# Optimization experiments

Hardware: AMD Instinct MI355X
Metric: run time of the kernel (lower is better)

Reference implementation:

```python
import jax, jax.numpy as jnp
import numpy as np

N_NODES = 50000
N_EDGES = 400000
H, D = 4, 32  # num_heads, per-head dim
NEG_SLOPE = 0.1


def setup_inputs() -> dict:
    key = jax.random.key(0)
    ks = jax.random.split(key, 12)
    inp = {
        'features': jax.random.normal(ks[0], (N_NODES, 256), jnp.float32) * 0.1,
        'src': jax.random.randint(ks[1], (N_EDGES,), 0, N_NODES, jnp.int32),
        'dst': jax.random.randint(ks[2], (N_EDGES,), 0, N_NODES, jnp.int32),
        'w': jax.random.uniform(ks[3], (N_EDGES,), jnp.float32),
        'W1': jax.random.normal(ks[4], (256, 128), jnp.float32) * 0.05,
        'al1': jax.random.normal(ks[5], (H, D), jnp.float32) * 0.1,
        'ar1': jax.random.normal(ks[6], (H, D), jnp.float32) * 0.1,
        'W2': jax.random.normal(ks[7], (128, 128), jnp.float32) * 0.05,
        'al2': jax.random.normal(ks[8], (H, D), jnp.float32) * 0.1,
        'ar2': jax.random.normal(ks[9], (H, D), jnp.float32) * 0.1,
        'Wout': jax.random.normal(ks[10], (256, 128), jnp.float32) * 0.05,
        'bout': jnp.zeros((128,), jnp.float32),
    }
    return inp


def _gat_layer(x, W, al, ar, src, dst, w):
    # x: [N, in_dim] -> ft: [N, H, D]
    ft = (x @ W).reshape(-1, H, D)
    el = jnp.einsum('nhd,hd->nh', ft, al)  # left attention logits per node
    er = jnp.einsum('nhd,hd->nh', ft, ar)
    # edge logits: leaky_relu(el[src] + er[dst]), then edge-weight scaling
    e = jax.nn.leaky_relu(el[src] + er[dst], negative_slope=NEG_SLOPE)  # [E, H]
    e = w[:, None] * e
    # segment softmax over incoming edges of each destination node
    m = jax.ops.segment_max(e, dst, num_segments=N_NODES)  # [N, H]
    a = jnp.exp(e - m[dst])
    s = jax.ops.segment_sum(a, dst, num_segments=N_NODES)
    a = a / s[dst]  # [E, H]
    # weighted scatter-sum aggregation: rst[dst] += a * ft[src]
    msg = ft[src] * a[:, :, None]  # [E, H, D]
    rst = jax.ops.segment_sum(msg, dst, num_segments=N_NODES)  # [N, H, D]
    # activation=relu, then concat heads (contiguous -> reshape)
    return jax.nn.relu(rst).reshape(-1, H * D)


def reference(features, src, dst, w, W1, al1, ar1, W2, al2, ar2, Wout, bout):
    x1 = _gat_layer(features, W1, al1, ar1, src, dst, w)  # [N, 128]
    x2 = _gat_layer(x1, W2, al2, ar2, src, dst, w)        # [N, 128]
    h = jnp.concatenate([x1, x2], axis=-1)                # [N, 256]
    return h @ Wout + bout                                # [N, 128]
```

## Files before the change

kernel.cpp:

```cpp
#include <hip/hip_runtime.h>
#include <math.h>

#define NHEAD 4
#define HDIM 32
#define NEG_SLOPE 0.1f

typedef unsigned short u16;
typedef unsigned int u32;
typedef _Float16 f16;
typedef f16 f16x2 __attribute__((ext_vector_type(2)));
typedef f16 f16x4 __attribute__((ext_vector_type(4)));
typedef f16 f16x8 __attribute__((ext_vector_type(8)));
typedef float f32x4 __attribute__((ext_vector_type(4)));

#define GLLDS16(g, l) __builtin_amdgcn_global_load_lds( \
    (const __attribute__((address_space(1))) void*)(g), \
    (__attribute__((address_space(3))) void*)(l), 16, 0, 0)


__device__ __forceinline__ void cast_panel(const float* __restrict__ W,
                                           const float* __restrict__ al,
                                           const float* __restrict__ ar,
                                           u16* __restrict__ bp, int t, int NC) {
    int per_kt = NC * 16;
    int kt = t / per_kt;
    int rem = t - kt * per_kt;
    int n = rem >> 4;
    int kkp = rem & 15;
    int k = kt * 32 + kkp * 2;
    float v0 = 0.f, v1 = 0.f;
    if (n < 128) {
        v0 = W[(size_t)k * 128 + n];
        v1 = W[(size_t)(k + 1) * 128 + n];
    } else if (n < 136) {
        const float* av = (n < 132) ? al : ar;
        int h = (n < 132) ? (n - 128) : (n - 132);
        float s0 = 0.f, s1 = 0.f;
        for (int d = 0; d < 32; d++) {
            float a = av[h * 32 + d];
            s0 += W[(size_t)k * 128 + h * 32 + d] * a;
            s1 += W[(size_t)(k + 1) * 128 + h * 32 + d] * a;
        }
        v0 = s0; v1 = s1;
    }
    f16x2 p;
    p.x = (f16)v0; p.y = (f16)v1;
    *(f16x2*)&((u32*)bp)[t] = p;
}

__global__ void histcast_k(const int* __restrict__ dst, int* __restrict__ cnt, int E,
                           const float* __restrict__ W1, const float* __restrict__ al1,
                           const float* __restrict__ ar1, u16* __restrict__ b1,
                           const float* __restrict__ W2, const float* __restrict__ al2,
                           const float* __restrict__ ar2, u16* __restrict__ b2,
                           const float* __restrict__ W3, u16* __restrict__ b3) {
    int t = blockIdx.x * 256 + threadIdx.x;
    if (t < E) atomicAdd(&cnt[dst[t]], 1);
    if (t < 18432) cast_panel(W1, al1, ar1, b1, t, 144);
    else if (t < 27648) cast_panel(W2, al2, ar2, b2, t - 18432, 144);
    else if (t < 44032) cast_panel(W3, nullptr, nullptr, b3, t - 27648, 128);
}


__global__ void assign_k(const int* __restrict__ cnt, int* __restrict__ start,
                         int* __restrict__ ctr, int N) {
    __shared__ int s[256];
    __shared__ int base;
    int t = threadIdx.x;
    int i = blockIdx.x * 256 + t;
    int v = (i < N) ? cnt[i] : 0;
    s[t] = v;
    __syncthreads();
    int incl = v;
    for (int off = 1; off < 256; off <<= 1) {
        int add = (t >= off) ? s[t - off] : 0;
        __syncthreads();
        incl += add;
        s[t] = incl;
        __syncthreads();
    }
    if (t == 255) base = atomicAdd(ctr, incl);
    __syncthreads();
    if (i < N) start[i] = base + incl - v;
}

__global__ void scatter_k(const int* __restrict__ src, const int* __restrict__ dst,
                          const float* __restrict__ w, const int* __restrict__ start,
                          int* __restrict__ fill, int2* __restrict__ edge_s, int E) {
    int e = blockIdx.x * 256 + threadIdx.x;
    if (e >= E) return;
    int d = dst[e];
    int p = atomicAdd(&fill[d], 1);
    edge_s[start[d] + p] = make_int2(src[e], __float_as_int(w[e]));
}


template <int NT>
__global__ __launch_bounds__(256) void gemm_h_k(
        const void* __restrict__ Av, int a_is_f16, int lda,
        const u16* __restrict__ Bp,
        const float* __restrict__ bias, float* __restrict__ Cf,
        u16* __restrict__ Ch, float* __restrict__ el, float* __restrict__ er,
        int M, int K) {
    __shared__ u16 As[2048];
    __shared__ u16 Bs[NT * 512];
    int tid = threadIdx.x;
    int w = tid >> 6, lane = tid & 63;
    int row0 = blockIdx.x * 64;
    int mrow = lane & 15;
    int koff = (lane >> 4) * 8;

    f32x4 acc[NT];
#pragma unroll
    for (int nt = 0; nt < NT; nt++) acc[nt] = (f32x4){0.f, 0.f, 0.f, 0.f};

    for (int k0 = 0; k0 < K; k0 += 32) {
        int kt = k0 >> 5;
#pragma unroll
        for (int i = 0; i < (NT * 64 + 255) / 256; i++) {
            int c = tid + i * 256;
            if (c < NT * 64)
                GLLDS16(Bp + (size_t)kt * (NT * 512) + (size_t)c * 8, &Bs[c * 8]);
        }
        if (a_is_f16) {
            const u16* Ah = (const u16*)Av;
            int c = tid;
            int r = c >> 2, kk = (c & 3) << 3;
            GLLDS16(Ah + (size_t)(row0 + r) * lda + k0 + kk, &As[c * 8]);
        } else {
            const float* Af = (const float*)Av;
#pragma unroll
            for (int i = 0; i < 2; i++) {
                int flat = tid + i * 256;
                int r = flat >> 3, c4 = flat & 7;
                int row = min(row0 + r, M - 1);
                float4 v = *(const float4*)&Af[(size_t)row * lda + k0 + c4 * 4];
                f16x4 p;
                p.x = (f16)v.x; p.y = (f16)v.y; p.z = (f16)v.z; p.w = (f16)v.w;
                *(f16x4*)&As[r * 32 + c4 * 4] = p;
            }
        }
        __syncthreads();

        f16x8 ah = *(const f16x8*)&As[(w * 16 + mrow) * 32 + koff];
#pragma unroll
        for (int nt = 0; nt < NT; nt++) {
            f16x8 bh = *(const f16x8*)&Bs[(nt * 16 + mrow) * 32 + koff];
            acc[nt] = __builtin_amdgcn_mfma_f32_16x16x32_f16(ah, bh, acc[nt], 0, 0, 0);
        }
        __syncthreads();
    }

    int rbase = row0 + w * 16 + (lane >> 4) * 4;
#pragma unroll
    for (int nt = 0; nt < 8; nt++) {
        int col = nt * 16 + mrow;
        float bv = bias ? bias[col] : 0.f;
        f32x4 v = acc[nt];
#pragma unroll
        for (int reg = 0; reg < 4; reg++) {
            int rr = rbase + reg;
            if (rr < M) {
                float val = v[reg] + bv;
                if (Cf) Cf[(size_t)rr * 128 + col] = val;
                if (Ch) *(f16*)&Ch[(size_t)rr * 128 + col] = (f16)val;
            }
        }
    }
    if (NT == 9) {
        f32x4 v = acc[8];
#pragma unroll
        for (int reg = 0; reg < 4; reg++) {
            int rr = rbase + reg;
            if (rr < M) {
                if (mrow < 4) el[rr * 4 + mrow] = v[reg];
                else if (mrow < 8) er[rr * 4 + (mrow - 4)] = v[reg];
            }
        }
    }
}


__device__ __forceinline__ float lrelu(float x) {
    return x > 0.f ? x : NEG_SLOPE * x;
}

__global__ __launch_bounds__(256) void agg_k(const u32* __restrict__ fth2,
                                             const float4* __restrict__ el4,
                                             const float4* __restrict__ er4,
                                             const int2* __restrict__ edge_s,
                                             const int* __restrict__ start,
                                             const int* __restrict__ cnt,
                                             u16* __restrict__ xcat,
                                             int ooff, int N) {
    __shared__ float4 sA[256];
    __shared__ int sS[256];
    int wv = threadIdx.x >> 6;
    int n = blockIdx.x * 4 + wv;
    if (n >= N) return;
    int lane = threadIdx.x & 63;
    int head = lane >> 4;
    int r0 = start[n], deg = cnt[n];
    u16* op = &xcat[(size_t)n * 256 + ooff + 2 * lane];
    if (deg == 0) {
        *(u32*)op = 0;
        return;
    }
    float4 ern = er4[n];
    float acc0 = 0.f, acc1 = 0.f;
    if (deg <= 64) {
        float4 a = make_float4(0.f, 0.f, 0.f, 0.f);
        int s = 0;
        if (lane < deg) {
            int2 ep = edge_s[r0 + lane];
            s = ep.x;
            float we = __int_as_float(ep.y);
            float4 e = el4[s];
            a.x = __expf(we * lrelu(e.x + ern.x));
            a.y = __expf(we * lrelu(e.y + ern.y));
            a.z = __expf(we * lrelu(e.z + ern.z));
            a.w = __expf(we * lrelu(e.w + ern.w));
        }
        float4 sm = a;
        for (int m = 1; m < deg; m <<= 1) {
            sm.x += __shfl_xor(sm.x, m);
            sm.y += __shfl_xor(sm.y, m);
            sm.z += __shfl_xor(sm.z, m);
            sm.w += __shfl_xor(sm.w, m);
        }
        a.x = a.x / sm.x; a.y = a.y / sm.y;
        a.z = a.z / sm.z; a.w = a.w / sm.w;
        sA[wv * 64 + lane] = a;
        sS[wv * 64 + lane] = s;
        const float* sAf = (const float*)&sA[wv * 64];
        const int* sSp = &sS[wv * 64];
        int i = 0;
        for (; i + 8 <= deg; i += 8) {
            float wg[8];
            u32 pp[8];
#pragma unroll
            for (int j = 0; j < 8; j++) {
                wg[j] = sAf[(i + j) * 4 + head];
                pp[j] = fth2[(size_t)sSp[i + j] * 64 + lane];
            }
#pragma unroll
            for (int j = 0; j < 8; j++) {
                f16x2 hp = *(const f16x2*)&pp[j];
                acc0 += wg[j] * (float)hp.x;
                acc1 += wg[j] * (float)hp.y;
            }
        }
        for (; i < deg; i++) {
            float wgt = sAf[i * 4 + head];
            u32 p = fth2[(size_t)sSp[i] * 64 + lane];
            f16x2 hp = *(const f16x2*)&p;
            acc0 += wgt * (float)hp.x;
            acc1 += wgt * (float)hp.y;
        }
    } else {
        float4 mx = make_float4(-INFINITY, -INFINITY, -INFINITY, -INFINITY);
        for (int i = lane; i < deg; i += 64) {
            int2 ep = edge_s[r0 + i];
            float we = __int_as_float(ep.y);
            float4 e = el4[ep.x];
            mx.x = fmaxf(mx.x, we * lrelu(e.x + ern.x));
            mx.y = fmaxf(mx.y, we * lrelu(e.y + ern.y));
            mx.z = fmaxf(mx.z, we * lrelu(e.z + ern.z));
            mx.w = fmaxf(mx.w, we * lrelu(e.w + ern.w));
        }
        for (int m = 32; m >= 1; m >>= 1) {
            mx.x = fmaxf(mx.x, __shfl_xor(mx.x, m));
            mx.y = fmaxf(mx.y, __shfl_xor(mx.y, m));
            mx.z = fmaxf(mx.z, __shfl_xor(mx.z, m));
            mx.w = fmaxf(mx.w, __shfl_xor(mx.w, m));
        }
        float4 sm = make_float4(0.f, 0.f, 0.f, 0.f);
        for (int i = lane; i < deg; i += 64) {
            int2 ep = edge_s[r0 + i];
            float we = __int_as_float(ep.y);
            float4 e = el4[ep.x];
            sm.x += __expf(we * lrelu(e.x + ern.x) - mx.x);
            sm.y += __expf(we * lrelu(e.y + ern.y) - mx.y);
            sm.z += __expf(we * lrelu(e.z + ern.z) - mx.z);
            sm.w += __expf(we * lrelu(e.w + ern.w) - mx.w);
        }
        for (int m = 32; m >= 1; m >>= 1) {
            sm.x += __shfl_xor(sm.x, m);
            sm.y += __shfl_xor(sm.y, m);
            sm.z += __shfl_xor(sm.z, m);
            sm.w += __shfl_xor(sm.w, m);
        }
        float4 inv;
        inv.x = 1.f / sm.x; inv.y = 1.f / sm.y;
        inv.z = 1.f / sm.z; inv.w = 1.f / sm.w;
        for (int i = 0; i < deg; i++) {
            int2 ep = edge_s[r0 + i];
            int si = ep.x;
            float we = __int_as_float(ep.y);
            float4 e = el4[si];
            float ax = __expf(we * lrelu(e.x + ern.x) - mx.x) * inv.x;
            float ay = __expf(we * lrelu(e.y + ern.y) - mx.y) * inv.y;
            float az = __expf(we * lrelu(e.z + ern.z) - mx.z) * inv.z;
            float aw = __expf(we * lrelu(e.w + ern.w) - mx.w) * inv.w;
            float wgt = head == 0 ? ax : (head == 1 ? ay : (head == 2 ? az : aw));
            u32 p = fth2[(size_t)si * 64 + lane];
            f16x2 hp = *(const f16x2*)&p;
            acc0 += wgt * (float)hp.x;
            acc1 += wgt * (float)hp.y;
        }
    }
    f16x2 hv;
    hv.x = (f16)fmaxf(acc0, 0.f);
    hv.y = (f16)fmaxf(acc1, 0.f);
    *(f16x2*)op = hv;
}


extern "C" void kernel_launch(void* const* d_in, const int* in_sizes, int n_in,
                              void* d_out, int out_size, void* d_ws, size_t ws_size,
                              hipStream_t stream) {
    const float* features = (const float*)d_in[0];
    const int* src = (const int*)d_in[1];
    const int* dst = (const int*)d_in[2];
    const float* w = (const float*)d_in[3];
    const float* W1 = (const float*)d_in[4];
    const float* al1 = (const float*)d_in[5];
    const float* ar1 = (const float*)d_in[6];
    const float* W2 = (const float*)d_in[7];
    const float* al2 = (const float*)d_in[8];
    const float* ar2 = (const float*)d_in[9];
    const float* Wout = (const float*)d_in[10];
    const float* bout = (const float*)d_in[11];
    float* out = (float*)d_out;

    int N = in_sizes[0] / 256;
    int E = in_sizes[1];
    int Mpad = ((N + 127) / 128) * 128;

    char* ws = (char*)d_ws;
    size_t off = 0;
    auto alloc = [&](size_t bytes) -> void* {
        void* p = ws + off;
        off = (off + bytes + 255) & ~(size_t)255;
        return p;
    };
    size_t Nr = ((size_t)N * 4 + 255) & ~(size_t)255;
    int* cnt = (int*)alloc(2 * Nr + 256);
    int* fill = (int*)((char*)cnt + Nr);
    int* ctr = (int*)((char*)cnt + 2 * Nr);
    int* start = (int*)alloc((size_t)N * 4);
    int2* edge_s = (int2*)alloc((size_t)E * 8);
    u16* fth = (u16*)alloc((size_t)Mpad * 128 * 2);
    float* el = (float*)alloc((size_t)N * 4 * 4);
    float* er = (float*)alloc((size_t)N * 4 * 4);
    u16* xcat = (u16*)alloc((size_t)Mpad * 256 * 2);
    u16* b1 = (u16*)alloc((size_t)18432 * 4);
    u16* b2 = (u16*)alloc((size_t)9216 * 4);
    u16* b3 = (u16*)alloc((size_t)16384 * 4);
    (void)ws_size; (void)n_in; (void)out_size;

    hipMemsetAsync(cnt, 0, 2 * Nr + 256, stream);

    int eb = (E + 255) / 256;
    int nb = (N + 255) / 256;
    int wb = (N + 3) / 4;
    int gb = Mpad / 64;

    histcast_k<<<eb, 256, 0, stream>>>(dst, cnt, E, W1, al1, ar1, b1,
                                       W2, al2, ar2, b2, Wout, b3);
    assign_k<<<nb, 256, 0, stream>>>(cnt, start, ctr, N);
    scatter_k<<<eb, 256, 0, stream>>>(src, dst, w, start, fill, edge_s, E);

    gemm_h_k<9><<<gb, 256, 0, stream>>>(features, 0, 256, b1, nullptr,
                                        nullptr, fth, el, er, N, 256);
    agg_k<<<wb, 256, 0, stream>>>((const u32*)fth, (const float4*)el, (const float4*)er,
                                  edge_s, start, cnt, xcat, 0, N);

    gemm_h_k<9><<<gb, 256, 0, stream>>>(xcat, 1, 256, b2, nullptr,
                                        nullptr, fth, el, er, N, 128);
    agg_k<<<wb, 256, 0, stream>>>((const u32*)fth, (const float4*)el, (const float4*)er,
                                  edge_s, start, cnt, xcat, 128, N);

    gemm_h_k<8><<<gb, 256, 0, stream>>>(xcat, 1, 256, b3, bout,
                                        out, nullptr, nullptr, nullptr, N, 256);
}
```

Baseline: 260.0 us.

## Preload full B panel into LDS and double-buffer A tiles in GEMM

The GEMM kernel now loads the whole weight panel for all K tiles into LDS once at kernel start, and double-buffers the A tile. The next A tile is prefetched, into registers for fp32 input or via direct global-to-LDS loads for fp16, while the MFMAs run on the current tile. This removes per-iteration B reloads and one barrier per K step, and the K loop is fully unrolled via a template parameter. In exchange, LDS use grows to up to about 74 KB per block for NT=9, KT=8, which can cut occupancy.

Result: slower. 283.6 us (+9.1%).

```diff
diff --git a/kernel.cpp b/kernel.cpp
--- a/kernel.cpp
+++ b/kernel.cpp
@@ -95,58 +95,86 @@
 }
 
 
-template <int NT>
+template <int NT, int KT>
 __global__ __launch_bounds__(256) void gemm_h_k(
         const void* __restrict__ Av, int a_is_f16, int lda,
         const u16* __restrict__ Bp,
         const float* __restrict__ bias, float* __restrict__ Cf,
         u16* __restrict__ Ch, float* __restrict__ el, float* __restrict__ er,
-        int M, int K) {
-    __shared__ u16 As[2048];
-    __shared__ u16 Bs[NT * 512];
+        int M) {
+    __shared__ u16 Bs[KT * NT * 512];
+    __shared__ u16 As[2][2048];
     int tid = threadIdx.x;
     int w = tid >> 6, lane = tid & 63;
     int row0 = blockIdx.x * 64;
     int mrow = lane & 15;
     int koff = (lane >> 4) * 8;
 
+    const u16* Ah = (const u16*)Av;
+    const float* Af = (const float*)Av;
+
+#pragma unroll
+    for (int i = 0; i < KT * NT * 64 / 256; i++) {
+        int c = tid + i * 256;
+        GLLDS16(Bp + (size_t)c * 8, &Bs[c * 8]);
+    }
+    if (a_is_f16) {
+        int c = tid;
+        GLLDS16(Ah + (size_t)(row0 + (c >> 2)) * lda + ((c & 3) << 3), &As[0][c * 8]);
+    } else {
+#pragma unroll
+        for (int i = 0; i < 2; i++) {
+            int flat = tid + i * 256;
+            int r = flat >> 3, c4 = flat & 7;
+            int row = min(row0 + r, M - 1);
+            float4 v = *(const float4*)&Af[(size_t)row * lda + c4 * 4];
+            f16x4 p;
+            p.x = (f16)v.x; p.y = (f16)v.y; p.z = (f16)v.z; p.w = (f16)v.w;
+            *(f16x4*)&As[0][r * 32 + c4 * 4] = p;
+        }
+    }
+    __syncthreads();
+
     f32x4 acc[NT];
 #pragma unroll
     for (int nt = 0; nt < NT; nt++) acc[nt] = (f32x4){0.f, 0.f, 0.f, 0.f};
 
-    for (int k0 = 0; k0 < K; k0 += 32) {
-        int kt = k0 >> 5;
-#pragma unroll
-        for (int i = 0; i < (NT * 64 + 255) / 256; i++) {
-            int c = tid + i * 256;
-            if (c < NT * 64)
-                GLLDS16(Bp + (size_t)kt * (NT * 512) + (size_t)c * 8, &Bs[c * 8]);
-        }
-        if (a_is_f16) {
-            const u16* Ah = (const u16*)Av;
-            int c = tid;
-            int r = c >> 2, kk = (c & 3) << 3;
-            GLLDS16(Ah + (size_t)(row0 + r) * lda + k0 + kk, &As[c * 8]);
-        } else {
-            const float* Af = (const float*)Av;
+    float4 pv[2];
+#pragma unroll
+    for (int kt = 0; kt < KT; kt++) {
+        int cur = kt & 1, nxt = cur ^ 1;
+        int k0n = (kt + 1) * 32;
+        if (kt + 1 < KT) {
+            if (a_is_f16) {
+                int c = tid;
+                GLLDS16(Ah + (size_t)(row0 + (c >> 2)) * lda + k0n + ((c & 3) << 3),
+                        &As[nxt][c * 8]);
+            } else {
+#pragma unroll
+                for (int i = 0; i < 2; i++) {
+                    int flat = tid + i * 256;
+                    int r = flat >> 3, c4 = flat & 7;
+                    int row = min(row0 + r, M - 1);
+                    pv[i] = *(const float4*)&Af[(size_t)row * lda + k0n + c4 * 4];
+                }
+            }
+        }
+        f16x8 ah = *(const f16x8*)&As[cur][(w * 16 + mrow) * 32 + koff];
+#pragma unroll
+        for (int nt = 0; nt < NT; nt++) {
+            f16x8 bh = *(const f16x8*)&Bs[(kt * NT + nt) * 512 + mrow * 32 + koff];
+            acc[nt] = __builtin_amdgcn_mfma_f32_16x16x32_f16(ah, bh, acc[nt], 0, 0, 0);
+        }
+        if (kt + 1 < KT && !a_is_f16) {
 #pragma unroll
             for (int i = 0; i < 2; i++) {
                 int flat = tid + i * 256;
                 int r = flat >> 3, c4 = flat & 7;
-                int row = min(row0 + r, M - 1);
-                float4 v = *(const float4*)&Af[(size_t)row * lda + k0 + c4 * 4];
                 f16x4 p;
-                p.x = (f16)v.x; p.y = (f16)v.y; p.z = (f16)v.z; p.w = (f16)v.w;
-                *(f16x4*)&As[r * 32 + c4 * 4] = p;
-            }
-        }
-        __syncthreads();
-
-        f16x8 ah = *(const f16x8*)&As[(w * 16 + mrow) * 32 + koff];
-#pragma unroll
-        for (int nt = 0; nt < NT; nt++) {
-            f16x8 bh = *(const f16x8*)&Bs[(nt * 16 + mrow) * 32 + koff];
-            acc[nt] = __builtin_amdgcn_mfma_f32_16x16x32_f16(ah, bh, acc[nt], 0, 0, 0);
+                p.x = (f16)pv[i].x; p.y = (f16)pv[i].y;
+                p.z = (f16)pv[i].z; p.w = (f16)pv[i].w;
+                *(f16x4*)&As[nxt][r * 32 + c4 * 4] = p;
+            }
         }
         __syncthreads();
     }
@@ -371,16 +399,16 @@
     assign_k<<<nb, 256, 0, stream>>>(cnt, start, ctr, N);
     scatter_k<<<eb, 256, 0, stream>>>(src, dst, w, start, fill, edge_s, E);
 
-    gemm_h_k<9><<<gb, 256, 0, stream>>>(features, 0, 256, b1, nullptr,
-                                        nullptr, fth, el, er, N, 256);
+    gemm_h_k<9, 8><<<gb, 256, 0, stream>>>(features, 0, 256, b1, nullptr,
+                                           nullptr, fth, el, er, N);
     agg_k<<<wb, 256, 0, stream>>>((const u32*)fth, (const float4*)el, (const float4*)er,
                                   edge_s, start, cnt, xcat, 0, N);
 
-    gemm_h_k<9><<<gb, 256, 0, stream>>>(xcat, 1, 256, b2, nullptr,
-                                        nullptr, fth, el, er, N, 128);
+    gemm_h_k<9, 4><<<gb, 256, 0, stream>>>(xcat, 1, 256, b2, nullptr,
+                                           nullptr, fth, el, er, N);
     agg_k<<<wb, 256, 0, stream>>>((const u32*)fth, (const float4*)el, (const float4*)er,
                                   edge_s, start, cnt, xcat, 128, N);
 
-    gemm_h_k<8><<<gb, 256, 0, stream>>>(xcat, 1, 256, b3, bout,
-                                        out, nullptr, nullptr, nullptr, N, 256);
-}
+    gemm_h_k<8, 8><<<gb, 256, 0, stream>>>(xcat, 1, 256, b3, bout,
+                                           out, nullptr, nullptr, nullptr, N);
+}
```
